# Kernel optimization log

Hardware: AMD Instinct MI355X
Metric: run time of the kernel (lower is better)

The kernel has to match this reference:

```python
import jax, jax.numpy as jnp
import numpy as np

N, E, D, H = 4096, 131072, 256, 8
HD = D // H
NEG_INF = -1e30  # stand-in for float('-inf'); avoids inf-inf NaN issues, softmax identical


def _linear(x, W, b):
    return x @ W + b


def setup_inputs() -> dict:
    key = jax.random.key(0)
    ks = jax.random.split(key, 16)
    s = 1.0 / np.sqrt(D)
    inp = {
        "x": jax.random.normal(ks[0], (N, D), jnp.float32),
        "edge_index": jax.random.randint(ks[1], (2, E), 0, N, jnp.int32),
        "edge_attr": jax.random.normal(ks[2], (E, D), jnp.float32),
        "Wq": jax.random.normal(ks[3], (D, D), jnp.float32) * s,
        "bq": jnp.zeros((D,), jnp.float32),
        "Wk": jax.random.normal(ks[4], (D, D), jnp.float32) * s,
        "bk": jnp.zeros((D,), jnp.float32),
        "Wv": jax.random.normal(ks[5], (D, D), jnp.float32) * s,
        "bv": jnp.zeros((D,), jnp.float32),
        "We": jax.random.normal(ks[6], (D, D), jnp.float32) * s,
        "be": jnp.zeros((D,), jnp.float32),
        "Wo": jax.random.normal(ks[7], (D, D), jnp.float32) * s,
        "bo": jnp.zeros((D,), jnp.float32),
        "Wi": jax.random.normal(ks[8], (D, D), jnp.float32) * s,
        "bi": jnp.zeros((D,), jnp.float32),
        "ln_g": jnp.ones((D,), jnp.float32),
        "ln_b": jnp.zeros((D,), jnp.float32),
    }
    return inp


def reference(x, edge_index, edge_attr, Wq, bq, Wk, bk, Wv, bv, We, be, Wo, bo, Wi, bi, ln_g, ln_b):
    n, e = x.shape[0], edge_attr.shape[0]
    Q = _linear(x, Wq, bq).reshape(n, H, HD)
    K = _linear(x, Wk, bk).reshape(n, H, HD)
    V = _linear(x, Wv, bv).reshape(n, H, HD)
    Efeat = _linear(edge_attr, We, be).reshape(e, H, HD)

    src, tgt = edge_index[0], edge_index[1]
    Q_src = Q[src]                     # (E, H, HD)
    K_tgt = K[tgt]                     # (E, H, HD)
    attn_edge = ((Q_src * K_tgt).sum(-1)
                 + (Q_src * Efeat).sum(-1)
                 + (Efeat * K_tgt).sum(-1)) / np.sqrt(HD)   # (E, H)

    attn_scores = jnp.full((n, n, H), NEG_INF, jnp.float32)
    attn_scores = attn_scores.at[src, tgt].set(attn_edge)
    attn_self = (Q * K).sum(-1) / np.sqrt(HD)               # (N, H)
    ar = jnp.arange(n)
    attn_scores = attn_scores.at[ar, ar].set(attn_self)

    attn_weights = jax.nn.softmax(attn_scores, axis=1)      # (N, N, H)
    # dropout in eval mode: identity
    node_out = jnp.einsum('ijh,jhd->ihd', attn_weights, V).reshape(n, -1)
    node_out = _linear(node_out, Wo, bo)

    x_proj = _linear(x, Wi, bi)
    h = x_proj + node_out
    mu = h.mean(-1, keepdims=True)
    var = ((h - mu) ** 2).mean(-1, keepdims=True)
    node_out = (h - mu) / jnp.sqrt(var + 1e-5) * ln_g + ln_b

    edge_out = _linear(edge_attr, We, be)
    return node_out, edge_out
```

## Files before the change

kernel.cpp:

```cpp
#include <hip/hip_runtime.h>

#define N_NODES 4096
#define N_EDGES 131072
#define DIM     256
#define HEADS   8
#define HDIM    32
#define MAXDEG  320
#define MAXDEGP 321

typedef unsigned short u16;
typedef unsigned int   u32;

using f32x4  = __attribute__((ext_vector_type(4))) float;
using bf16x8 = __attribute__((ext_vector_type(8))) short;
using u16x4  = __attribute__((ext_vector_type(4))) unsigned short;
using u16x8  = __attribute__((ext_vector_type(8))) unsigned short;

__device__ __forceinline__ u16 f2bf(float f) {
  u32 u = __float_as_uint(f);
  u += 0x7fffu + ((u >> 16) & 1u);
  return (u16)(u >> 16);
}
__device__ __forceinline__ float bf2f(u16 u) {
  return __uint_as_float(((u32)u) << 16);
}
__device__ __forceinline__ float dot4(float4 a, float4 b) {
  return a.x * b.x + a.y * b.y + a.z * b.z + a.w * b.w;
}

__global__ __launch_bounds__(256) void prep_w_k(
    const float* __restrict__ Wq, const float* __restrict__ Wk,
    const float* __restrict__ Wv, const float* __restrict__ Wi,
    const float* __restrict__ We, const float* __restrict__ Wo,
    const float* __restrict__ bq, const float* __restrict__ bk,
    const float* __restrict__ bv, const float* __restrict__ bi,
    u16* __restrict__ WcatT, u16* __restrict__ WeT, u16* __restrict__ WoT,
    float* __restrict__ bcat, int* __restrict__ deg)
{
  int n = blockIdx.x;
  int k = threadIdx.x;
  if (n < 1024) {
    const float* W = (n < 256) ? Wq : (n < 512) ? Wk : (n < 768) ? Wv : Wi;
    int nn = n & 255;
    WcatT[(size_t)n * 256 + k] = f2bf(W[(size_t)k * 256 + nn]);
    if (k == 0) {
      const float* b = (n < 256) ? bq : (n < 512) ? bk : (n < 768) ? bv : bi;
      bcat[n] = b[nn];
    }
  } else if (n < 1280) {
    int nn = n - 1024;
    WeT[(size_t)nn * 256 + k] = f2bf(We[(size_t)k * 256 + nn]);
  } else if (n < 1536) {
    int nn = n - 1280;
    WoT[(size_t)nn * 256 + k] = f2bf(Wo[(size_t)k * 256 + nn]);
  } else {
    deg[(n - 1536) * 256 + k] = 0;
  }
}

template<int MODE>
__device__ __forceinline__ void gemm_big_body(
    const float* __restrict__ A, const u16* __restrict__ BT,
    const float* __restrict__ bias, float* __restrict__ C, int Nn,
    int m0, int nc0,
    u16* __restrict__ Kb, u16* __restrict__ Vb,
    const float* __restrict__ QKVI, const float* __restrict__ lng,
    const float* __restrict__ lnb, float* __restrict__ outN,
    u16 (&As)[2][128 * 32], u16 (&Bs)[2][256 * 32])
{
  const int tid = threadIdx.x;
  const int w = tid >> 6, l = tid & 63;
  const int wr = w >> 2, wc = w & 3;
  const int fr = l & 15, hi = l >> 4;

  f32x4 pa[2];
  u16x8 pb[2];
  f32x4 acc[4][4] = {};

  auto loadstep = [&](int kt) {
#pragma unroll
    for (int i = 0; i < 2; ++i) {
      int j = tid + 512 * i;
      pa[i] = __builtin_nontemporal_load(
          (const f32x4*)(A + (size_t)(m0 + (j >> 3)) * 256 + kt * 32 + ((j & 7) << 2)));
    }
#pragma unroll
    for (int i = 0; i < 2; ++i) {
      int j = tid + 512 * i;
      pb[i] = *(const u16x8*)(BT + (size_t)(nc0 + (j >> 2)) * 256 + kt * 32 + ((j & 3) << 3));
    }
  };
  auto storestep = [&](int buf) {
#pragma unroll
    for (int i = 0; i < 2; ++i) {
      int j = tid + 512 * i;
      int row = j >> 3;
      int c16 = (j & 7) >> 1, half = j & 1;
      int swc = (c16 + ((row >> 1) & 3)) & 3;
      u16x4 u;
      u.x = f2bf(pa[i][0]); u.y = f2bf(pa[i][1]); u.z = f2bf(pa[i][2]); u.w = f2bf(pa[i][3]);
      *(u16x4*)&As[buf][row * 32 + swc * 8 + half * 4] = u;
    }
#pragma unroll
    for (int i = 0; i < 2; ++i) {
      int j = tid + 512 * i;
      int row = j >> 2;
      int swc = ((j & 3) + ((row >> 1) & 3)) & 3;
      *(u16x8*)&Bs[buf][row * 32 + swc * 8] = pb[i];
    }
  };

  loadstep(0);
  storestep(0);

#pragma unroll
  for (int kt = 0; kt < 8; ++kt) {
    if (kt < 7) loadstep(kt + 1);
    __builtin_amdgcn_sched_barrier(0);
    asm volatile("s_waitcnt lgkmcnt(0)" ::: "memory");
    __builtin_amdgcn_s_barrier();
    __builtin_amdgcn_sched_barrier(0);
    const int cur = kt & 1;
    bf16x8 a[4], b[4];
#pragma unroll
    for (int mi = 0; mi < 4; ++mi) {
      int rA = wr * 64 + mi * 16 + fr;
      int swc = (hi + ((rA >> 1) & 3)) & 3;
      a[mi] = *(const bf16x8*)&As[cur][rA * 32 + swc * 8];
    }
#pragma unroll
    for (int ni = 0; ni < 4; ++ni) {
      int rB = wc * 64 + ni * 16 + fr;
      int swc = (hi + ((rB >> 1) & 3)) & 3;
      b[ni] = *(const bf16x8*)&Bs[cur][rB * 32 + swc * 8];
    }
#pragma unroll
    for (int mi = 0; mi < 4; ++mi)
#pragma unroll
      for (int ni = 0; ni < 4; ++ni)
        acc[mi][ni] = __builtin_amdgcn_mfma_f32_16x16x32_bf16(
            b[ni], a[mi], acc[mi][ni], 0, 0, 0);
    if (kt < 7) storestep((kt + 1) & 1);
  }

  if constexpr (MODE == 0) {
#pragma unroll
    for (int mi = 0; mi < 4; ++mi) {
      int row = m0 + wr * 64 + mi * 16 + fr;
#pragma unroll
      for (int ni = 0; ni < 4; ++ni) {
        int col = wc * 64 + ni * 16 + hi * 4;
        float4 bv = *(const float4*)&bias[col];
        f32x4 v = acc[mi][ni];
        float4 o;
        o.x = v[0] + bv.x; o.y = v[1] + bv.y; o.z = v[2] + bv.z; o.w = v[3] + bv.w;
        *(float4*)&C[(size_t)row * 256 + col] = o;
      }
    }
  } else if constexpr (MODE == 1) {
#pragma unroll
    for (int mi = 0; mi < 4; ++mi) {
      int row = m0 + wr * 64 + mi * 16 + fr;
#pragma unroll
      for (int ni = 0; ni < 4; ++ni) {
        int col = nc0 + wc * 64 + ni * 16 + hi * 4;
        float4 bv = *(const float4*)&bias[col];
        f32x4 v = acc[mi][ni];
        float4 o;
        o.x = v[0] + bv.x; o.y = v[1] + bv.y; o.z = v[2] + bv.z; o.w = v[3] + bv.w;
        *(float4*)&C[(size_t)row * 1024 + col] = o;
        u16x4 ub;
        ub.x = f2bf(o.x); ub.y = f2bf(o.y); ub.z = f2bf(o.z); ub.w = f2bf(o.w);
        if (nc0 == 256) *(u16x4*)&Kb[(size_t)row * 256 + (col - 256)] = ub;
        if (nc0 == 512) *(u16x4*)&Vb[(size_t)row * 256 + (col - 512)] = ub;
      }
    }
  } else {
    __syncthreads();
    float* s_sum = (float*)&As[0][0];
    float* s_sq  = (float*)&As[1][0];
#pragma unroll
    for (int mi = 0; mi < 4; ++mi) {
      int r = wr * 64 + mi * 16 + fr;
      int row = m0 + r;
      float ps = 0.f, pq = 0.f;
#pragma unroll
      for (int ni = 0; ni < 4; ++ni) {
        int col = wc * 64 + ni * 16 + hi * 4;
        float4 bv = *(const float4*)&bias[col];
        float4 xp = *(const float4*)&QKVI[(size_t)row * 1024 + 768 + col];
        acc[mi][ni][0] += bv.x + xp.x;
        acc[mi][ni][1] += bv.y + xp.y;
        acc[mi][ni][2] += bv.z + xp.z;
        acc[mi][ni][3] += bv.w + xp.w;
#pragma unroll
        for (int j = 0; j < 4; ++j) {
          float vv = acc[mi][ni][j];
          ps += vv; pq += vv * vv;
        }
      }
      s_sum[r * 16 + wc * 4 + hi] = ps;
      s_sq [r * 16 + wc * 4 + hi] = pq;
    }
    __syncthreads();
    float* s_mu = (float*)&Bs[0][0];
    float* s_rs = s_mu + 128;
    if (tid < 128) {
      float s = 0.f, q = 0.f;
#pragma unroll
      for (int k = 0; k < 16; ++k) { s += s_sum[tid * 16 + k]; q += s_sq[tid * 16 + k]; }
      float mu = s * (1.0f / 256.0f);
      float var = q * (1.0f / 256.0f) - mu * mu;
      s_mu[tid] = mu;
      s_rs[tid] = rsqrtf(var + 1e-5f);
    }
    __syncthreads();
#pragma unroll
    for (int mi = 0; mi < 4; ++mi) {
      int r = wr * 64 + mi * 16 + fr;
      int row = m0 + r;
      float mu = s_mu[r], rs = s_rs[r];
#pragma unroll
      for (int ni = 0; ni < 4; ++ni) {
        int col = wc * 64 + ni * 16 + hi * 4;
        float4 g4 = *(const float4*)&lng[col];
        float4 b4 = *(const float4*)&lnb[col];
        float4 o;
        o.x = (acc[mi][ni][0] - mu) * rs * g4.x + b4.x;
        o.y = (acc[mi][ni][1] - mu) * rs * g4.y + b4.y;
        o.z = (acc[mi][ni][2] - mu) * rs * g4.z + b4.z;
        o.w = (acc[mi][ni][3] - mu) * rs * g4.w + b4.w;
        *(float4*)&outN[(size_t)row * 256 + col] = o;
      }
    }
  }
}

__global__ __launch_bounds__(512) void gemm_all_k(
    const float* __restrict__ ea, const u16* __restrict__ WeT,
    const float* __restrict__ be, float* __restrict__ outE,
    const float* __restrict__ x, const u16* __restrict__ WcatT,
    const float* __restrict__ bcat, float* __restrict__ QKVI,
    u16* __restrict__ Kb, u16* __restrict__ Vb)
{
  __shared__ u16 As[2][128 * 32];
  __shared__ u16 Bs[2][256 * 32];
  int bid = blockIdx.x;
  int r = bid % 9, q = bid / 9;
  if (r < 8) {
    int j = q * 8 + r;
    gemm_big_body<0>(ea, WeT, be, outE, 256, j * 128, 0,
                     nullptr, nullptr, nullptr, nullptr, nullptr, nullptr, As, Bs);
  } else {
    gemm_big_body<1>(x, WcatT, bcat, QKVI, 1024, (q >> 2) * 128, (q & 3) * 256,
                     Kb, Vb, nullptr, nullptr, nullptr, nullptr, As, Bs);
  }
}

__global__ __launch_bounds__(512) void gemm_wo_k(
    const float* __restrict__ agg, const u16* __restrict__ WoT,
    const float* __restrict__ bo, const float* __restrict__ QKVI,
    const float* __restrict__ lng, const float* __restrict__ lnb,
    float* __restrict__ outN)
{
  __shared__ u16 As[2][128 * 32];
  __shared__ u16 Bs[2][256 * 32];
  gemm_big_body<2>(agg, WoT, bo, nullptr, 256, blockIdx.x * 128, 0,
                   nullptr, nullptr, QKVI, lng, lnb, outN, As, Bs);
}

__global__ __launch_bounds__(256) void hist_k(const int* __restrict__ src, int* __restrict__ deg)
{
  int e = blockIdx.x * 256 + threadIdx.x;
  if (e < N_EDGES) atomicAdd(&deg[src[e]], 1);
}

__global__ __launch_bounds__(1024) void scan_k(const int* __restrict__ deg,
                                               int* __restrict__ rowstart,
                                               int* __restrict__ cursor)
{
  __shared__ int s[1024];
  int tid = threadIdx.x;
  int4 v = ((const int4*)deg)[tid];
  int sum = v.x + v.y + v.z + v.w;
  s[tid] = sum;
  __syncthreads();
  for (int off = 1; off < 1024; off <<= 1) {
    int t = (tid >= off) ? s[tid - off] : 0;
    __syncthreads();
    s[tid] += t;
    __syncthreads();
  }
  int excl = s[tid] - sum;
  int r0 = excl, r1 = excl + v.x, r2 = r1 + v.y, r3 = r2 + v.z;
  rowstart[4 * tid + 0] = r0; cursor[4 * tid + 0] = r0;
  rowstart[4 * tid + 1] = r1; cursor[4 * tid + 1] = r1;
  rowstart[4 * tid + 2] = r2; cursor[4 * tid + 2] = r2;
  rowstart[4 * tid + 3] = r3; cursor[4 * tid + 3] = r3;
  if (tid == 1023) rowstart[4096] = r3 + v.w;
}

__global__ __launch_bounds__(256) void scatter_k(const int* __restrict__ src,
                                                 int* __restrict__ cursor,
                                                 int* __restrict__ csr)
{
  int e = blockIdx.x * 256 + threadIdx.x;
  if (e < N_EDGES) {
    int p = atomicAdd(&cursor[src[e]], 1);
    csr[p] = e;
  }
}

__global__ __launch_bounds__(256) void node_attn_k(
    const float* __restrict__ QKVI, const float* __restrict__ Ef,
    const u16* __restrict__ Kb, const u16* __restrict__ Vb,
    const int* __restrict__ rowstart, const int* __restrict__ csr,
    const int* __restrict__ tgt, float* __restrict__ agg)
{
  __shared__ int   s_eid[MAXDEG];
  __shared__ int   s_tgt[MAXDEG];
  __shared__ float s_sc[HEADS][MAXDEGP];
  __shared__ unsigned char s_alive[MAXDEG];
  __shared__ float s_self[8];
  __shared__ float s_wself[8];

  const float scl = 0.17677669529663687f;
  int i = blockIdx.x;
  int base = rowstart[i];
  int deg = rowstart[i + 1] - base;
  if (deg > MAXDEG) deg = MAXDEG;
  int tid = threadIdx.x;
  int w = tid >> 6, l = tid & 63;
  int h = tid >> 5, d = tid & 31;

  for (int t = tid; t < deg; t += 256) {
    int e = csr[base + t];
    s_eid[t] = e;
    s_tgt[t] = tgt[e];
  }
  __syncthreads();

  float4 q4 = *(const float4*)&QKVI[(size_t)i * 1024 + 4 * l];

  if (w == 0) {
    u16x4 kb = *(const u16x4*)&Kb[(size_t)i * 256 + 4 * l];
    float4 k4 = make_float4(bf2f(kb.x), bf2f(kb.y), bf2f(kb.z), bf2f(kb.w));
    float c = dot4(q4, k4);
    c += __shfl_xor(c, 1); c += __shfl_xor(c, 2); c += __shfl_xor(c, 4);
    if ((l & 7) == 0) s_self[l >> 3] = c * scl;
  }

  for (int t0 = w; t0 < deg; t0 += 16) {
    float4 ef[4], k4[4];
#pragma unroll
    for (int u = 0; u < 4; ++u) {
      int t = t0 + 4 * u;
      if (t < deg) {
        ef[u] = *(const float4*)&Ef[(size_t)s_eid[t] * 256 + 4 * l];
        u16x4 kb = *(const u16x4*)&Kb[(size_t)s_tgt[t] * 256 + 4 * l];
        k4[u] = make_float4(bf2f(kb.x), bf2f(kb.y), bf2f(kb.z), bf2f(kb.w));
      }
    }
#pragma unroll
    for (int u = 0; u < 4; ++u) {
      int t = t0 + 4 * u;
      if (t < deg) {
        float c = dot4(q4, ef[u]) + dot4(ef[u], k4[u]) + dot4(q4, k4[u]);
        c += __shfl_xor(c, 1); c += __shfl_xor(c, 2); c += __shfl_xor(c, 4);
        if ((l & 7) == 0) s_sc[l >> 3][t] = c * scl;
      }
    }
  }

  for (int t = tid; t < deg; t += 256) {
    int tt = s_tgt[t], ee = s_eid[t];
    bool alive = (tt != i);
    if (alive)
      for (int u = 0; u < deg; ++u)
        if (s_tgt[u] == tt && s_eid[u] > ee) { alive = false; break; }
    s_alive[t] = alive ? 1 : 0;
  }
  __syncthreads();

  {
    float m = s_self[h];
    for (int t = d; t < deg; t += 32)
      if (s_alive[t]) m = fmaxf(m, s_sc[h][t]);
#pragma unroll
    for (int off = 16; off > 0; off >>= 1) m = fmaxf(m, __shfl_xor(m, off, 32));
    float lsum = 0.f;
    for (int t = d; t < deg; t += 32) {
      float wv = s_alive[t] ? expf(s_sc[h][t] - m) : 0.f;
      s_sc[h][t] = wv;
      lsum += wv;
    }
#pragma unroll
    for (int off = 16; off > 0; off >>= 1) lsum += __shfl_xor(lsum, off, 32);
    float wself = expf(s_self[h] - m);
    float inv = 1.f / (lsum + wself);
    if (d == 0) s_wself[h] = wself * inv;
    for (int t = d; t < deg; t += 32) s_sc[h][t] *= inv;
  }
  __syncthreads();

  int col = tid;
  float accv = s_wself[h] * bf2f(Vb[(size_t)i * 256 + col]);
  int t0 = 0;
  for (; t0 + 4 <= deg; t0 += 4) {
    float vl[4];
#pragma unroll
    for (int u = 0; u < 4; ++u)
      vl[u] = bf2f(Vb[(size_t)s_tgt[t0 + u] * 256 + col]);
#pragma unroll
    for (int u = 0; u < 4; ++u)
      accv += s_sc[h][t0 + u] * vl[u];
  }
  for (; t0 < deg; ++t0)
    accv += s_sc[h][t0] * bf2f(Vb[(size_t)s_tgt[t0] * 256 + col]);
  agg[(size_t)i * 256 + col] = accv;
}

extern "C" void kernel_launch(void* const* d_in, const int* in_sizes, int n_in,
                              void* d_out, int out_size, void* d_ws, size_t ws_size,
                              hipStream_t stream) {
  (void)in_sizes; (void)n_in; (void)out_size; (void)ws_size;
  const float* x  = (const float*)d_in[0];
  const int*   ei = (const int*)d_in[1];
  const float* ea = (const float*)d_in[2];
  const float* Wq = (const float*)d_in[3];  const float* bq = (const float*)d_in[4];
  const float* Wk = (const float*)d_in[5];  const float* bk = (const float*)d_in[6];
  const float* Wv = (const float*)d_in[7];  const float* bv = (const float*)d_in[8];
  const float* We = (const float*)d_in[9];  const float* be = (const float*)d_in[10];
  const float* Wo = (const float*)d_in[11]; const float* bo = (const float*)d_in[12];
  const float* Wi = (const float*)d_in[13]; const float* bi = (const float*)d_in[14];
  const float* lng = (const float*)d_in[15]; const float* lnb = (const float*)d_in[16];

  const int* src = ei;
  const int* tgt = ei + N_EDGES;

  char* ws = (char*)d_ws;
  u16*   WcatT   = (u16*)(ws + 0);
  u16*   WeT     = (u16*)(ws + 524288);
  u16*   WoT     = (u16*)(ws + 655360);
  float* bcat    = (float*)(ws + 786432);
  float* QKVI    = (float*)(ws + 790528);
  int*   deg     = (int*)(ws + 17567744);
  int*   rowstart= (int*)(ws + 17584128);
  int*   cursor  = (int*)(ws + 17600768);
  int*   csr     = (int*)(ws + 17617152);
  float* agg     = (float*)(ws + 18141440);
  u16*   Kb      = (u16*)(ws + 22335744);
  u16*   Vb      = (u16*)(ws + 24432896);

  float* outN = (float*)d_out;
  float* outE = (float*)d_out + (size_t)N_NODES * DIM;

  prep_w_k<<<1552, 256, 0, stream>>>(Wq, Wk, Wv, Wi, We, Wo, bq, bk, bv, bi,
                                     WcatT, WeT, WoT, bcat, deg);

  hist_k<<<N_EDGES / 256, 256, 0, stream>>>(src, deg);
  scan_k<<<1, 1024, 0, stream>>>(deg, rowstart, cursor);
  scatter_k<<<N_EDGES / 256, 256, 0, stream>>>(src, cursor, csr);

  gemm_all_k<<<1152, 512, 0, stream>>>(ea, WeT, be, outE, x, WcatT, bcat,
                                       QKVI, Kb, Vb);

  node_attn_k<<<N_NODES, 256, 0, stream>>>(QKVI, outE, Kb, Vb,
                                           rowstart, csr, tgt, agg);

  gemm_wo_k<<<N_NODES / 128, 512, 0, stream>>>(agg, WoT, bo, QKVI, lng, lnb, outN);
}
```

Before: 173.3 us.

## Replace CSR histogram/scan with fixed-capacity per-node slots; tile weight transpose

Drops the degree histogram and single-block prefix scan. Edges are scattered directly into fixed MAXDEG-sized per-node slot arrays using an atomic cursor, which then serves as the degree. The weight transpose/bf16 conversion now uses 64x64 shared-memory tiles for coalesced reads and writes, with far fewer blocks. This removes two kernel launches and a serialized scan, at the cost of a larger sparse slot buffer and strided slot reads.

```diff
diff --git a/kernel.cpp b/kernel.cpp
--- a/kernel.cpp
+++ b/kernel.cpp
@@ -28,33 +28,47 @@
   return a.x * b.x + a.y * b.y + a.z * b.z + a.w * b.w;
 }
 
-__global__ __launch_bounds__(256) void prep_w_k(
+__global__ __launch_bounds__(256) void prep2_k(
     const float* __restrict__ Wq, const float* __restrict__ Wk,
     const float* __restrict__ Wv, const float* __restrict__ Wi,
     const float* __restrict__ We, const float* __restrict__ Wo,
     const float* __restrict__ bq, const float* __restrict__ bk,
     const float* __restrict__ bv, const float* __restrict__ bi,
     u16* __restrict__ WcatT, u16* __restrict__ WeT, u16* __restrict__ WoT,
-    float* __restrict__ bcat, int* __restrict__ deg)
-{
-  int n = blockIdx.x;
-  int k = threadIdx.x;
-  if (n < 1024) {
-    const float* W = (n < 256) ? Wq : (n < 512) ? Wk : (n < 768) ? Wv : Wi;
-    int nn = n & 255;
-    WcatT[(size_t)n * 256 + k] = f2bf(W[(size_t)k * 256 + nn]);
-    if (k == 0) {
-      const float* b = (n < 256) ? bq : (n < 512) ? bk : (n < 768) ? bv : bi;
-      bcat[n] = b[nn];
-    }
-  } else if (n < 1280) {
-    int nn = n - 1024;
-    WeT[(size_t)nn * 256 + k] = f2bf(We[(size_t)k * 256 + nn]);
-  } else if (n < 1536) {
-    int nn = n - 1280;
-    WoT[(size_t)nn * 256 + k] = f2bf(Wo[(size_t)k * 256 + nn]);
+    float* __restrict__ bcat, int* __restrict__ cursor)
+{
+  __shared__ float t[64][65];
+  int b = blockIdx.x;
+  int tid = threadIdx.x;
+  if (b < 96) {
+    int mat = b >> 4, tile = b & 15;
+    int k0 = (tile >> 2) * 64, n0 = (tile & 3) * 64;
+    const float* W = (mat == 0) ? Wq : (mat == 1) ? Wk : (mat == 2) ? Wv
+                   : (mat == 3) ? Wi : (mat == 4) ? We : Wo;
+    u16* dst; int nbase;
+    if (mat < 4)      { dst = WcatT; nbase = mat * 256; }
+    else if (mat == 4){ dst = WeT;   nbase = 0; }
+    else              { dst = WoT;   nbase = 0; }
+    int c = tid & 63, r0 = tid >> 6;
+#pragma unroll
+    for (int r = 0; r < 16; ++r) {
+      int row = r0 + r * 4;
+      t[row][c] = W[(size_t)(k0 + row) * 256 + n0 + c];
+    }
+    __syncthreads();
+#pragma unroll
+    for (int r = 0; r < 16; ++r) {
+      int nn = r0 + r * 4;
+      dst[(size_t)(nbase + n0 + nn) * 256 + k0 + c] = f2bf(t[c][nn]);
+    }
+  } else if (b == 96) {
+#pragma unroll
+    for (int j = 0; j < 4; ++j) {
+      const float* bb = (j == 0) ? bq : (j == 1) ? bk : (j == 2) ? bv : bi;
+      bcat[j * 256 + tid] = bb[tid];
+    }
   } else {
-    deg[(n - 1536) * 256 + k] = 0;
+    ((int4*)cursor)[(b - 97) * 256 + tid] = make_int4(0, 0, 0, 0);
   }
 }
 
@@ -269,52 +283,22 @@
                    nullptr, nullptr, QKVI, lng, lnb, outN, As, Bs);
 }
 
-__global__ __launch_bounds__(256) void hist_k(const int* __restrict__ src, int* __restrict__ deg)
-{
-  int e = blockIdx.x * 256 + threadIdx.x;
-  if (e < N_EDGES) atomicAdd(&deg[src[e]], 1);
-}
-
-__global__ __launch_bounds__(1024) void scan_k(const int* __restrict__ deg,
-                                               int* __restrict__ rowstart,
-                                               int* __restrict__ cursor)
-{
-  __shared__ int s[1024];
-  int tid = threadIdx.x;
-  int4 v = ((const int4*)deg)[tid];
-  int sum = v.x + v.y + v.z + v.w;
-  s[tid] = sum;
-  __syncthreads();
-  for (int off = 1; off < 1024; off <<= 1) {
-    int t = (tid >= off) ? s[tid - off] : 0;
-    __syncthreads();
-    s[tid] += t;
-    __syncthreads();
-  }
-  int excl = s[tid] - sum;
-  int r0 = excl, r1 = excl + v.x, r2 = r1 + v.y, r3 = r2 + v.z;
-  rowstart[4 * tid + 0] = r0; cursor[4 * tid + 0] = r0;
-  rowstart[4 * tid + 1] = r1; cursor[4 * tid + 1] = r1;
-  rowstart[4 * tid + 2] = r2; cursor[4 * tid + 2] = r2;
-  rowstart[4 * tid + 3] = r3; cursor[4 * tid + 3] = r3;
-  if (tid == 1023) rowstart[4096] = r3 + v.w;
-}
-
 __global__ __launch_bounds__(256) void scatter_k(const int* __restrict__ src,
                                                  int* __restrict__ cursor,
-                                                 int* __restrict__ csr)
+                                                 int* __restrict__ slots)
 {
   int e = blockIdx.x * 256 + threadIdx.x;
   if (e < N_EDGES) {
-    int p = atomicAdd(&cursor[src[e]], 1);
-    csr[p] = e;
+    int s = src[e];
+    int p = atomicAdd(&cursor[s], 1);
+    if (p < MAXDEG) slots[(size_t)s * MAXDEG + p] = e;
   }
 }
 
 __global__ __launch_bounds__(256) void node_attn_k(
     const float* __restrict__ QKVI, const float* __restrict__ Ef,
     const u16* __restrict__ Kb, const u16* __restrict__ Vb,
-    const int* __restrict__ rowstart, const int* __restrict__ csr,
+    const int* __restrict__ cursor, const int* __restrict__ slots,
     const int* __restrict__ tgt, float* __restrict__ agg)
 {
   __shared__ int   s_eid[MAXDEG];
@@ -326,15 +310,14 @@
 
   const float scl = 0.17677669529663687f;
   int i = blockIdx.x;
-  int base = rowstart[i];
-  int deg = rowstart[i + 1] - base;
+  int deg = cursor[i];
   if (deg > MAXDEG) deg = MAXDEG;
   int tid = threadIdx.x;
   int w = tid >> 6, l = tid & 63;
   int h = tid >> 5, d = tid & 31;
 
   for (int t = tid; t < deg; t += 256) {
-    int e = csr[base + t];
+    int e = slots[(size_t)i * MAXDEG + t];
     s_eid[t] = e;
     s_tgt[t] = tgt[e];
   }
@@ -444,29 +427,25 @@
   u16*   WoT     = (u16*)(ws + 655360);
   float* bcat    = (float*)(ws + 786432);
   float* QKVI    = (float*)(ws + 790528);
-  int*   deg     = (int*)(ws + 17567744);
-  int*   rowstart= (int*)(ws + 17584128);
-  int*   cursor  = (int*)(ws + 17600768);
-  int*   csr     = (int*)(ws + 17617152);
-  float* agg     = (float*)(ws + 18141440);
-  u16*   Kb      = (u16*)(ws + 22335744);
-  u16*   Vb      = (u16*)(ws + 24432896);
+  int*   cursor  = (int*)(ws + 17567744);
+  int*   slots   = (int*)(ws + 17584128);
+  float* agg     = (float*)(ws + 22827008);
+  u16*   Kb      = (u16*)(ws + 27021312);
+  u16*   Vb      = (u16*)(ws + 29118464);
 
   float* outN = (float*)d_out;
   float* outE = (float*)d_out + (size_t)N_NODES * DIM;
 
-  prep_w_k<<<1552, 256, 0, stream>>>(Wq, Wk, Wv, Wi, We, Wo, bq, bk, bv, bi,
-                                     WcatT, WeT, WoT, bcat, deg);
-
-  hist_k<<<N_EDGES / 256, 256, 0, stream>>>(src, deg);
-  scan_k<<<1, 1024, 0, stream>>>(deg, rowstart, cursor);
-  scatter_k<<<N_EDGES / 256, 256, 0, stream>>>(src, cursor, csr);
+  prep2_k<<<101, 256, 0, stream>>>(Wq, Wk, Wv, Wi, We, Wo, bq, bk, bv, bi,
+                                   WcatT, WeT, WoT, bcat, cursor);
+
+  scatter_k<<<N_EDGES / 256, 256, 0, stream>>>(src, cursor, slots);
 
   gemm_all_k<<<1152, 512, 0, stream>>>(ea, WeT, be, outE, x, WcatT, bcat,
                                        QKVI, Kb, Vb);
 
   node_attn_k<<<N_NODES, 256, 0, stream>>>(QKVI, outE, Kb, Vb,
-                                           rowstart, csr, tgt, agg);
+                                           cursor, slots, tgt, agg);
 
   gemm_wo_k<<<N_NODES / 128, 512, 0, stream>>>(agg, WoT, bo, QKVI, lng, lnb, outN);
 }
```

Result: faster. 161.3 us, median of 2 (-7.0%).
